# Kernel optimization log

Hardware: AMD Instinct MI355X
Metric: run time of the kernel (lower is better)

Reference implementation:

```python
import jax, jax.numpy as jnp
import numpy as np

D = 1024
H = 16
DH = D // H  # 64
EPS = 1e-5


def _ln(x, w, b=None):
    mu = jnp.mean(x, axis=-1, keepdims=True)
    var = jnp.var(x, axis=-1, keepdims=True)
    y = (x - mu) * jax.lax.rsqrt(var + EPS) * w
    return y + b if b is not None else y


def _rotate_half(x):
    x1, x2 = jnp.split(x, 2, axis=-1)
    return jnp.concatenate([-x2, x1], axis=-1)


def _rope(q, k):
    # q, k: [B, L, H, DH]; rotary over sequence dim (ESM-style half-split rotation)
    L = q.shape[1]
    inv_freq = 1.0 / (10000.0 ** (jnp.arange(0, DH, 2, dtype=jnp.float32) / DH))
    freqs = jnp.arange(L, dtype=jnp.float32)[:, None] * inv_freq[None, :]  # [L, DH/2]
    emb = jnp.concatenate([freqs, freqs], axis=-1)  # [L, DH]
    cos = jnp.cos(emb)[None, :, None, :]  # [1, L, 1, DH]
    sin = jnp.sin(emb)[None, :, None, :]
    q = q * cos + _rotate_half(q) * sin
    k = k * cos + _rotate_half(k) * sin
    return q, k


def setup_inputs() -> dict:
    key = jax.random.key(0)
    ks = jax.random.split(key, 8)
    B, L = 2, 2048
    x = jax.random.normal(ks[0], (B, L, D), dtype=jnp.float32)
    seq_id = jnp.sort(jax.random.randint(ks[1], (B, L), 0, 8), axis=-1)
    s = 1.0 / np.sqrt(D)
    return {
        "x": x,
        "seq_id": seq_id,
        "ln1_w": jnp.ones((D,), jnp.float32),
        "ln1_b": jnp.zeros((D,), jnp.float32),
        "w_qkv": jax.random.normal(ks[2], (3 * D, D), dtype=jnp.float32) * s,
        "q_ln_w": jnp.ones((D,), jnp.float32),
        "k_ln_w": jnp.ones((D,), jnp.float32),
        "out_w": jax.random.normal(ks[3], (D, D), dtype=jnp.float32) * s,
    }


def reference(x, seq_id, ln1_w, ln1_b, w_qkv, q_ln_w, k_ln_w, out_w):
    B, L, _ = x.shape
    h = _ln(x, ln1_w, ln1_b)
    qkv = jnp.einsum("bld,ed->ble", h, w_qkv)  # [B, L, 3D]
    q, k, v = jnp.split(qkv, 3, axis=-1)
    q = _ln(q, q_ln_w)
    k = _ln(k, k_ln_w)
    q = q.reshape(B, L, H, DH)
    k = k.reshape(B, L, H, DH)
    q, k = _rope(q, k)
    q = q.transpose(0, 2, 1, 3)  # [B, H, L, DH]
    k = k.transpose(0, 2, 1, 3)
    v = v.reshape(B, L, H, DH).transpose(0, 2, 1, 3)
    scale = 1.0 / np.sqrt(DH)
    scores = jnp.einsum("bhld,bhmd->bhlm", q, k) * scale  # [B, H, L, L]
    mask = (seq_id[:, None, :, None] == seq_id[:, None, None, :])  # [B, 1, L, L]
    scores = jnp.where(mask, scores, -jnp.inf)
    attn = jax.nn.softmax(scores, axis=-1)
    ctx = jnp.einsum("bhlm,bhmd->bhld", attn, v)  # [B, H, L, DH]
    ctx = ctx.transpose(0, 2, 1, 3).reshape(B, L, D)
    return jnp.einsum("bld,ed->ble", ctx, out_w)
```

## Files before the change

kernel.cpp:

```cpp
#include <hip/hip_runtime.h>
#include <hip/hip_bf16.h>
#include <math.h>

#define D 1024
#define H 16
#define DH 64
#define L 2048
#define B 2
#define NROW (B * L)
#define EPS 1e-5f

typedef _Float16 half8 __attribute__((ext_vector_type(8)));
typedef _Float16 half4v __attribute__((ext_vector_type(4)));
typedef float f32x4 __attribute__((ext_vector_type(4)));

__global__ __launch_bounds__(256) void prep_kernel(const float* __restrict__ x,
                                                   const float* __restrict__ lw,
                                                   const float* __restrict__ lb,
                                                   _Float16* __restrict__ h16,
                                                   const float* __restrict__ wqkv,
                                                   _Float16* __restrict__ wqkv16,
                                                   const float* __restrict__ outw,
                                                   _Float16* __restrict__ outw16,
                                                   const int* __restrict__ seq_id,
                                                   int* __restrict__ lo,
                                                   int* __restrict__ hi,
                                                   float2* __restrict__ rtab) {
    int blk = blockIdx.x;
    int t = threadIdx.x;
    if (blk < 4096) {
        int r = blk;
        const float* xr = x + (size_t)r * D;
        float4 v = *(const float4*)&xr[t * 4];
        float s = v.x + v.y + v.z + v.w;
        float sq = v.x * v.x + v.y * v.y + v.z * v.z + v.w * v.w;
        for (int off = 32; off > 0; off >>= 1) {
            s += __shfl_xor(s, off, 64);
            sq += __shfl_xor(sq, off, 64);
        }
        __shared__ float ls[4], lq[4];
        int wave = t >> 6;
        if ((t & 63) == 0) { ls[wave] = s; lq[wave] = sq; }
        __syncthreads();
        float S = ls[0] + ls[1] + ls[2] + ls[3];
        float Q = lq[0] + lq[1] + lq[2] + lq[3];
        float mu = S / (float)D;
        float rs = rsqrtf(Q / (float)D - mu * mu + EPS);
        float4 w4 = *(const float4*)&lw[t * 4];
        float4 b4 = *(const float4*)&lb[t * 4];
        half4v o = {(_Float16)((v.x - mu) * rs * w4.x + b4.x),
                    (_Float16)((v.y - mu) * rs * w4.y + b4.y),
                    (_Float16)((v.z - mu) * rs * w4.z + b4.z),
                    (_Float16)((v.w - mu) * rs * w4.w + b4.w)};
        *(half4v*)&h16[(size_t)r * D + t * 4] = o;
    } else if (blk < 6144) {
        int base = blk - 4096;
        const float* src;
        _Float16* dst;
        if (base < 1536) { src = wqkv; dst = wqkv16; }
        else             { src = outw; dst = outw16; base -= 1536; }
        int i = (base * 256 + t) * 8;
        float4 a = *(const float4*)&src[i];
        float4 b = *(const float4*)&src[i + 4];
        half8 h = {(_Float16)a.x, (_Float16)a.y, (_Float16)a.z, (_Float16)a.w,
                   (_Float16)b.x, (_Float16)b.y, (_Float16)b.z, (_Float16)b.w};
        *(half8*)&dst[i] = h;
    } else if (blk < 6160) {
        int idx = (blk - 6144) * 256 + t;
        int b = idx / L, l = idx - b * L;
        const int* row = seq_id + (size_t)b * L;
        int v = row[l];
        int a = 0, c = L;
        while (a < c) { int m = (a + c) >> 1; if (row[m] < v) a = m + 1; else c = m; }
        lo[idx] = a;
        a = 0; c = L;
        while (a < c) { int m = (a + c) >> 1; if (row[m] <= v) a = m + 1; else c = m; }
        hi[idx] = a;
    } else {
        int idx = (blk - 6160) * 256 + t;
        int l = idx >> 5, fi = idx & 31;
        float invf = expf(-(float)fi * 0.28782313662425572f);
        float sn, cs;
        sincosf((float)l * invf, &sn, &cs);
        rtab[idx] = make_float2(cs, sn);
    }
}

template <typename OutT, int BM, int BN>
__global__ __launch_bounds__(256) void gemm_f16_kernel(const _Float16* __restrict__ A,
                                                       const _Float16* __restrict__ W,
                                                       OutT* __restrict__ C, int N) {
    constexpr int WM = BM / 2, WN = BN / 2;
    constexpr int MT = WM / 16, NT = WN / 16;
    __shared__ _Float16 As[2][BM * 32];
    __shared__ _Float16 Bs[2][BN * 32];
    int t = threadIdx.x;
    int w = t >> 6, lane = t & 63;
    int quad = lane >> 4, col = lane & 15;
    int m0 = blockIdx.y * BM, n0 = blockIdx.x * BN;
    int mw = (w >> 1) * WM, nw = (w & 1) * WN;
    int sw = (col >> 1) & 3;

    f32x4 acc[MT][NT] = {};

    auto stage = [&](int k0, int buf) {
#pragma unroll
        for (int i = 0; i < BM / 64; i++) {
            int e = t + i * 256;
            int row = e >> 2, kc = (e & 3) ^ ((row >> 1) & 3);
            __builtin_amdgcn_global_load_lds(
                (const __attribute__((address_space(1))) void*)&A[(size_t)(m0 + row) * 1024 + k0 + kc * 8],
                (__attribute__((address_space(3))) void*)&As[buf][e * 8], 16, 0, 0);
        }
#pragma unroll
        for (int i = 0; i < BN / 64; i++) {
            int e = t + i * 256;
            int row = e >> 2, kc = (e & 3) ^ ((row >> 1) & 3);
            __builtin_amdgcn_global_load_lds(
                (const __attribute__((address_space(1))) void*)&W[(size_t)(n0 + row) * 1024 + k0 + kc * 8],
                (__attribute__((address_space(3))) void*)&Bs[buf][e * 8], 16, 0, 0);
        }
    };

    stage(0, 0);
    int cur = 0;
    for (int k0 = 0; k0 < 1024; k0 += 32) {
        __syncthreads();
        if (k0 + 32 < 1024) stage(k0 + 32, cur ^ 1);
        half8 af[MT], bf[NT];
#pragma unroll
        for (int mt = 0; mt < MT; mt++)
            af[mt] = *(const half8*)&As[cur][(mw + mt * 16 + col) * 32 + ((quad ^ sw) << 3)];
#pragma unroll
        for (int nt = 0; nt < NT; nt++)
            bf[nt] = *(const half8*)&Bs[cur][(nw + nt * 16 + col) * 32 + ((quad ^ sw) << 3)];
#pragma unroll
        for (int mt = 0; mt < MT; mt++)
#pragma unroll
            for (int nt = 0; nt < NT; nt++)
                acc[mt][nt] = __builtin_amdgcn_mfma_f32_16x16x32_f16(af[mt], bf[nt], acc[mt][nt], 0, 0, 0);
        cur ^= 1;
    }

#pragma unroll
    for (int mt = 0; mt < MT; mt++)
#pragma unroll
        for (int nt = 0; nt < NT; nt++)
#pragma unroll
            for (int r = 0; r < 4; r++) {
                int row = m0 + mw + mt * 16 + quad * 4 + r;
                int cc = n0 + nw + nt * 16 + col;
                C[(size_t)row * N + cc] = (OutT)acc[mt][nt][r];
            }
}

__global__ __launch_bounds__(256) void mid_kernel(const _Float16* __restrict__ qkv,
                                                  const float* __restrict__ qw,
                                                  const float* __restrict__ kw,
                                                  const float2* __restrict__ rtab,
                                                  _Float16* __restrict__ q_r,
                                                  _Float16* __restrict__ k_r,
                                                  _Float16* __restrict__ v_t) {
    __shared__ float ls[4], lq[4];
    __shared__ _Float16 T[64][64];
    int blk = blockIdx.x;
    int t = threadIdx.x;
    if (blk < 8192) {
        int r = blk >> 1;
        int which = blk & 1;
        const _Float16* src = qkv + (size_t)r * 3072 + which * 1024;
        const float* w = which ? kw : qw;
        _Float16* dst = which ? k_r : q_r;

        float vals[4];
        float s = 0.f, sq = 0.f;
#pragma unroll
        for (int i = 0; i < 4; i++) {
            float v = (float)src[t + i * 256];
            vals[i] = v;
            s += v;
            sq += v * v;
        }
        for (int off = 32; off > 0; off >>= 1) {
            s += __shfl_xor(s, off, 64);
            sq += __shfl_xor(sq, off, 64);
        }
        int wave = t >> 6;
        if ((t & 63) == 0) { ls[wave] = s; lq[wave] = sq; }
        __syncthreads();
        float S = ls[0] + ls[1] + ls[2] + ls[3];
        float Q = lq[0] + lq[1] + lq[2] + lq[3];
        float mu = S / 1024.f;
        float rs = rsqrtf(Q / 1024.f - mu * mu + EPS);

        int l = r & (L - 1);
        int b = r >> 11;
#pragma unroll
        for (int i = 0; i < 4; i++) {
            int j = t + i * 256;
            float y = (vals[i] - mu) * rs * w[j];
            float p = __shfl_xor(y, 32, 64);
            int dh = j & 63, hh = j >> 6;
            float2 cs = rtab[l * 32 + (dh & 31)];
            float out = (dh < 32) ? (y * cs.x - p * cs.y) : (y * cs.x + p * cs.y);
            dst[((size_t)((b * H + hh) * L + l)) * 64 + dh] = (_Float16)out;
        }
    } else {
        int vb = blk - 8192;
        int bh = vb >> 5;
        int b = bh >> 4, h = bh & 15;
        int l0 = (vb & 31) * 64;
#pragma unroll
        for (int i = 0; i < 2; i++) {
            int e = t + i * 256;
            int li = e >> 3, ch = e & 7;
            half8 hv = *(const half8*)&qkv[((size_t)(b * L + l0 + li)) * 3072 + 2048 + h * 64 + ch * 8];
            *(half8*)&T[li][((ch ^ (li >> 3)) & 7) * 8] = hv;
        }
        __syncthreads();
#pragma unroll
        for (int i = 0; i < 2; i++) {
            int e = t + i * 256;
            int d = e >> 3, ch = e & 7;
            half8 hv;
#pragma unroll
            for (int j = 0; j < 8; j++)
                hv[j] = T[ch * 8 + j][((((d >> 3) ^ ch) & 7) * 8) + (d & 7)];
            *(half8*)&v_t[((size_t)(bh * 64 + d)) * 2048 + l0 + ch * 8] = hv;
        }
    }
}

__global__ __launch_bounds__(256) void attn_mfma_kernel(const _Float16* __restrict__ q_r,
                                                        const _Float16* __restrict__ k_r,
                                                        const _Float16* __restrict__ v_t,
                                                        const int* __restrict__ lo_arr,
                                                        const int* __restrict__ hi_arr,
                                                        _Float16* __restrict__ ctx) {
    __shared__ _Float16 Ks[2][64][64];
    __shared__ _Float16 Vs[2][64][64];
    __shared__ _Float16 Ps[4][16][64];
    int bh = blockIdx.y;
    int b = bh >> 4, h = bh & 15;
    int l0 = blockIdx.x * 64;
    int t = threadIdx.x;
    int w = t >> 6, lane = t & 63;
    int quad = lane >> 4, col = lane & 15;
    int rbase = l0 + w * 16;

    int blo = lo_arr[b * L + l0] & ~63;
    int bhi = hi_arr[b * L + l0 + 63];

    auto stage = [&](int m0, int buf) {
#pragma unroll
        for (int i = 0; i < 2; i++) {
            int e = t + i * 256;
            int row = e >> 3, ch = e & 7;
            int sch = ch ^ (row & 7);
            __builtin_amdgcn_global_load_lds(
                (const __attribute__((address_space(1))) void*)&k_r[((size_t)(bh * L + m0 + row)) * 64 + sch * 8],
                (__attribute__((address_space(3))) void*)&Ks[buf][row][ch * 8], 16, 0, 0);
            __builtin_amdgcn_global_load_lds(
                (const __attribute__((address_space(1))) void*)&v_t[((size_t)(bh * 64 + row)) * 2048 + m0 + sch * 8],
                (__attribute__((address_space(3))) void*)&Vs[buf][row][ch * 8], 16, 0, 0);
        }
    };

    stage(blo, 0);

    half8 qf0, qf1;
    {
        const _Float16* qp = q_r + ((size_t)(bh * L + rbase + col)) * 64 + quad * 8;
        qf0 = *(const half8*)qp;
        qf1 = *(const half8*)(qp + 32);
    }
    int lo_c = lo_arr[b * L + rbase + col];
    int hi_c = hi_arr[b * L + rbase + col];
    int wlo = __shfl(lo_c, 15, 64);
    int whi = __shfl(hi_c, 0, 64);

    f32x4 o[4] = {};
    float m_run = -1e30f, l_run = 0.f;
    const float SCL = 0.125f * 1.4426950408889634f;
    int swz = (col & 7) << 3;
    int src = (lane & 48) | ((lane & 48) >> 2);

    int cur = 0;
    for (int m0 = blo; m0 < bhi; m0 += 64) {
        __syncthreads();
        if (m0 + 64 < bhi) stage(m0 + 64, cur ^ 1);

        f32x4 s[4] = {};
#pragma unroll
        for (int nt = 0; nt < 4; nt++) {
            int key = nt * 16 + col;
            const _Float16* kp = &Ks[cur][key][0];
            half8 kf0 = *(const half8*)&kp[(quad ^ (key & 7)) * 8];
            half8 kf1 = *(const half8*)&kp[((quad + 4) ^ (key & 7)) * 8];
            s[nt] = __builtin_amdgcn_mfma_f32_16x16x32_f16(kf0, qf0, s[nt], 0, 0, 0);
            s[nt] = __builtin_amdgcn_mfma_f32_16x16x32_f16(kf1, qf1, s[nt], 0, 0, 0);
        }

        float p[4][4];
        bool full = (m0 >= wlo) && (m0 + 64 <= whi);
        if (full) {
#pragma unroll
            for (int nt = 0; nt < 4; nt++)
#pragma unroll
                for (int r = 0; r < 4; r++) p[nt][r] = s[nt][r] * SCL;
        } else {
#pragma unroll
            for (int nt = 0; nt < 4; nt++) {
                int kb = m0 + nt * 16 + quad * 4;
#pragma unroll
                for (int r = 0; r < 4; r++) {
                    int key = kb + r;
                    p[nt][r] = (key >= lo_c && key < hi_c) ? s[nt][r] * SCL : -INFINITY;
                }
            }
        }

        float tmax = p[0][0];
#pragma unroll
        for (int nt = 0; nt < 4; nt++)
#pragma unroll
            for (int r = 0; r < 4; r++) tmax = fmaxf(tmax, p[nt][r]);
        tmax = fmaxf(tmax, __shfl_xor(tmax, 16, 64));
        tmax = fmaxf(tmax, __shfl_xor(tmax, 32, 64));
        float nm = fmaxf(m_run, tmax);
        float corr = exp2f(m_run - nm);
        m_run = nm;
        float rs = 0.f;
#pragma unroll
        for (int nt = 0; nt < 4; nt++)
#pragma unroll
            for (int r = 0; r < 4; r++) {
                float e2 = exp2f(p[nt][r] - nm);
                p[nt][r] = e2;
                rs += e2;
            }
        rs += __shfl_xor(rs, 16, 64);
        rs += __shfl_xor(rs, 32, 64);
        l_run = l_run * corr + rs;

#pragma unroll
        for (int nt = 0; nt < 4; nt++) {
            half4v pk = {(_Float16)p[nt][0], (_Float16)p[nt][1],
                         (_Float16)p[nt][2], (_Float16)p[nt][3]};
            *(half4v*)&Ps[w][col][(nt * 16 + quad * 4) ^ swz] = pk;
        }

#pragma unroll
        for (int r = 0; r < 4; r++) {
            float c4 = __shfl(corr, src + r, 64);
            o[0][r] *= c4; o[1][r] *= c4; o[2][r] *= c4; o[3][r] *= c4;
        }

        half8 pf0 = *(const half8*)&Ps[w][col][(quad * 8) ^ swz];
        half8 pf1 = *(const half8*)&Ps[w][col][(32 + quad * 8) ^ swz];
#pragma unroll
        for (int nt = 0; nt < 4; nt++) {
            int dr = nt * 16 + col;
            const _Float16* vp = &Vs[cur][dr][0];
            half8 vf0 = *(const half8*)&vp[(quad ^ (dr & 7)) * 8];
            half8 vf1 = *(const half8*)&vp[((quad + 4) ^ (dr & 7)) * 8];
            o[nt] = __builtin_amdgcn_mfma_f32_16x16x32_f16(pf0, vf0, o[nt], 0, 0, 0);
            o[nt] = __builtin_amdgcn_mfma_f32_16x16x32_f16(pf1, vf1, o[nt], 0, 0, 0);
        }
        cur ^= 1;
    }

#pragma unroll
    for (int r = 0; r < 4; r++) {
        float linv = 1.f / __shfl(l_run, src + r, 64);
        int row = rbase + quad * 4 + r;
#pragma unroll
        for (int nt = 0; nt < 4; nt++)
            ctx[((size_t)(b * L + row)) * 1024 + h * 64 + nt * 16 + col] =
                (_Float16)(o[nt][r] * linv);
    }
}

extern "C" void kernel_launch(void* const* d_in, const int* in_sizes, int n_in,
                              void* d_out, int out_size, void* d_ws, size_t ws_size,
                              hipStream_t stream) {
    const float* x      = (const float*)d_in[0];
    const int*   seq_id = (const int*)d_in[1];
    const float* ln1_w  = (const float*)d_in[2];
    const float* ln1_b  = (const float*)d_in[3];
    const float* w_qkv  = (const float*)d_in[4];
    const float* q_ln_w = (const float*)d_in[5];
    const float* k_ln_w = (const float*)d_in[6];
    const float* out_w  = (const float*)d_in[7];
    float* out = (float*)d_out;

    char* ws = (char*)d_ws;
    int*      lo     = (int*)(ws);
    int*      hi     = (int*)(ws + (64 << 10));
    float2*   rtab   = (float2*)(ws + (128 << 10));
    _Float16* h16    = (_Float16*)(ws + (1ull << 20));
    _Float16* wqkv16 = (_Float16*)(ws + (10ull << 20));
    _Float16* outw16 = (_Float16*)(ws + (17ull << 20));
    _Float16* qkv16  = (_Float16*)(ws + (20ull << 20));
    _Float16* q_r    = (_Float16*)(ws + (45ull << 20));
    _Float16* k_r    = (_Float16*)(ws + (54ull << 20));
    _Float16* v_t    = (_Float16*)(ws + (63ull << 20));
    _Float16* ctx16  = (_Float16*)(ws + (72ull << 20));

    prep_kernel<<<dim3(6416), dim3(256), 0, stream>>>(
        x, ln1_w, ln1_b, h16, w_qkv, wqkv16, out_w, outw16, seq_id, lo, hi, rtab);
    gemm_f16_kernel<_Float16, 128, 128><<<dim3(3072 / 128, NROW / 128), dim3(256), 0, stream>>>(
        h16, wqkv16, qkv16, 3072);
    mid_kernel<<<dim3(9216), dim3(256), 0, stream>>>(qkv16, q_ln_w, k_ln_w, rtab, q_r, k_r, v_t);
    attn_mfma_kernel<<<dim3(L / 64, B * H), dim3(256), 0, stream>>>(q_r, k_r, v_t, lo, hi, ctx16);
    gemm_f16_kernel<float, 128, 64><<<dim3(1024 / 64, NROW / 128), dim3(256), 0, stream>>>(
        ctx16, outw16, out, 1024);

    (void)in_sizes; (void)n_in; (void)out_size; (void)ws_size;
}
```

Measured before the change: 190.2 us.

## Remap GEMM tiles across XCDs, vectorize q/k norm-rope, enlarge attention blocks

The GEMM kernel remaps its flat block index so consecutive tiles go to the same XCD (stride-8 interleave), aiming at better L2 reuse. The q/k layernorm plus rotary kernel now handles one row's q and k per block with 8-wide vector loads and stores, using a lane shuffle of 4 for the rotate-half pairing. The attention kernel moves to 512 threads covering 128 query rows per block, so each staged K/V tile serves twice as many queries. The cost is fewer attention blocks and a wider key range per block, which means more masked work at segment boundaries.

```diff
diff --git a/kernel.cpp b/kernel.cpp
--- a/kernel.cpp
+++ b/kernel.cpp
@@ -97,7 +97,11 @@
     int t = threadIdx.x;
     int w = t >> 6, lane = t & 63;
     int quad = lane >> 4, col = lane & 15;
-    int m0 = blockIdx.y * BM, n0 = blockIdx.x * BN;
+    int nx = gridDim.x;
+    int ib = blockIdx.y * nx + blockIdx.x;
+    int nwg = nx * gridDim.y;
+    int ni = (ib & 7) * (nwg >> 3) + (ib >> 3);
+    int m0 = (ni / nx) * BM, n0 = (ni % nx) * BN;
     int mw = (w >> 1) * WM, nw = (w & 1) * WN;
     int sw = (col >> 1) & 3;
 
@@ -165,19 +169,21 @@
     __shared__ _Float16 T[64][64];
     int blk = blockIdx.x;
     int t = threadIdx.x;
-    if (blk < 8192) {
-        int r = blk >> 1;
-        int which = blk & 1;
-        const _Float16* src = qkv + (size_t)r * 3072 + which * 1024;
-        const float* w = which ? kw : qw;
-        _Float16* dst = which ? k_r : q_r;
-
-        float vals[4];
+    if (blk < 4096) {
+        int r = blk;
+        int half = t >> 7;
+        int tt = t & 127;
+        const _Float16* src = qkv + (size_t)r * 3072 + half * 1024;
+        const float* wgt = half ? kw : qw;
+        _Float16* dst = half ? k_r : q_r;
+
+        half8 hv = *(const half8*)&src[tt * 8];
+        float y[8];
         float s = 0.f, sq = 0.f;
 #pragma unroll
-        for (int i = 0; i < 4; i++) {
-            float v = (float)src[t + i * 256];
-            vals[i] = v;
+        for (int e = 0; e < 8; e++) {
+            float v = (float)hv[e];
+            y[e] = v;
             s += v;
             sq += v * v;
         }
@@ -188,25 +194,37 @@
         int wave = t >> 6;
         if ((t & 63) == 0) { ls[wave] = s; lq[wave] = sq; }
         __syncthreads();
-        float S = ls[0] + ls[1] + ls[2] + ls[3];
-        float Q = lq[0] + lq[1] + lq[2] + lq[3];
+        int base = half << 1;
+        float S = ls[base] + ls[base + 1];
+        float Q = lq[base] + lq[base + 1];
         float mu = S / 1024.f;
         float rs = rsqrtf(Q / 1024.f - mu * mu + EPS);
 
         int l = r & (L - 1);
         int b = r >> 11;
-#pragma unroll
-        for (int i = 0; i < 4; i++) {
-            int j = t + i * 256;
-            float y = (vals[i] - mu) * rs * w[j];
-            float p = __shfl_xor(y, 32, 64);
-            int dh = j & 63, hh = j >> 6;
-            float2 cs = rtab[l * 32 + (dh & 31)];
-            float out = (dh < 32) ? (y * cs.x - p * cs.y) : (y * cs.x + p * cs.y);
-            dst[((size_t)((b * H + hh) * L + l)) * 64 + dh] = (_Float16)out;
-        }
+        int j0 = tt * 8;
+        int dh0 = j0 & 63, hh = j0 >> 6;
+        const float2* cp = &rtab[l * 32 + (dh0 & 31)];
+        float4 c01 = *(const float4*)cp;
+        float4 c23 = *(const float4*)(cp + 2);
+        float4 c45 = *(const float4*)(cp + 4);
+        float4 c67 = *(const float4*)(cp + 6);
+        float cs_[8] = {c01.x, c01.z, c23.x, c23.z, c45.x, c45.z, c67.x, c67.z};
+        float sn_[8] = {c01.y, c01.w, c23.y, c23.w, c45.y, c45.w, c67.y, c67.w};
+
+        float yn[8];
+#pragma unroll
+        for (int e = 0; e < 8; e++) yn[e] = (y[e] - mu) * rs * wgt[j0 + e];
+        float sgn = (dh0 < 32) ? -1.f : 1.f;
+        half8 o;
+#pragma unroll
+        for (int e = 0; e < 8; e++) {
+            float p = __shfl_xor(yn[e], 4, 64);
+            o[e] = (_Float16)(yn[e] * cs_[e] + sgn * p * sn_[e]);
+        }
+        *(half8*)&dst[((size_t)((b * H + hh) * L + l)) * 64 + dh0] = o;
     } else {
-        int vb = blk - 8192;
+        int vb = blk - 4096;
         int bh = vb >> 5;
         int b = bh >> 4, h = bh & 15;
         int l0 = (vb & 31) * 64;
@@ -231,7 +249,7 @@
     }
 }
 
-__global__ __launch_bounds__(256) void attn_mfma_kernel(const _Float16* __restrict__ q_r,
+__global__ __launch_bounds__(512) void attn_mfma_kernel(const _Float16* __restrict__ q_r,
                                                         const _Float16* __restrict__ k_r,
                                                         const _Float16* __restrict__ v_t,
                                                         const int* __restrict__ lo_arr,
@@ -239,31 +257,27 @@
                                                         _Float16* __restrict__ ctx) {
     __shared__ _Float16 Ks[2][64][64];
     __shared__ _Float16 Vs[2][64][64];
-    __shared__ _Float16 Ps[4][16][64];
+    __shared__ _Float16 Ps[8][16][64];
     int bh = blockIdx.y;
     int b = bh >> 4, h = bh & 15;
-    int l0 = blockIdx.x * 64;
+    int l0 = blockIdx.x * 128;
     int t = threadIdx.x;
     int w = t >> 6, lane = t & 63;
     int quad = lane >> 4, col = lane & 15;
     int rbase = l0 + w * 16;
 
     int blo = lo_arr[b * L + l0] & ~63;
-    int bhi = hi_arr[b * L + l0 + 63];
+    int bhi = hi_arr[b * L + l0 + 127];
 
     auto stage = [&](int m0, int buf) {
-#pragma unroll
-        for (int i = 0; i < 2; i++) {
-            int e = t + i * 256;
-            int row = e >> 3, ch = e & 7;
-            int sch = ch ^ (row & 7);
-            __builtin_amdgcn_global_load_lds(
-                (const __attribute__((address_space(1))) void*)&k_r[((size_t)(bh * L + m0 + row)) * 64 + sch * 8],
-                (__attribute__((address_space(3))) void*)&Ks[buf][row][ch * 8], 16, 0, 0);
-            __builtin_amdgcn_global_load_lds(
-                (const __attribute__((address_space(1))) void*)&v_t[((size_t)(bh * 64 + row)) * 2048 + m0 + sch * 8],
-                (__attribute__((address_space(3))) void*)&Vs[buf][row][ch * 8], 16, 0, 0);
-        }
+        int row = t >> 3, ch = t & 7;
+        int sch = ch ^ (row & 7);
+        __builtin_amdgcn_global_load_lds(
+            (const __attribute__((address_space(1))) void*)&k_r[((size_t)(bh * L + m0 + row)) * 64 + sch * 8],
+            (__attribute__((address_space(3))) void*)&Ks[buf][row][ch * 8], 16, 0, 0);
+        __builtin_amdgcn_global_load_lds(
+            (const __attribute__((address_space(1))) void*)&v_t[((size_t)(bh * 64 + row)) * 2048 + m0 + sch * 8],
+            (__attribute__((address_space(3))) void*)&Vs[buf][row][ch * 8], 16, 0, 0);
     };
 
     stage(blo, 0);
@@ -411,8 +425,8 @@
         x, ln1_w, ln1_b, h16, w_qkv, wqkv16, out_w, outw16, seq_id, lo, hi, rtab);
     gemm_f16_kernel<_Float16, 128, 128><<<dim3(3072 / 128, NROW / 128), dim3(256), 0, stream>>>(
         h16, wqkv16, qkv16, 3072);
-    mid_kernel<<<dim3(9216), dim3(256), 0, stream>>>(qkv16, q_ln_w, k_ln_w, rtab, q_r, k_r, v_t);
-    attn_mfma_kernel<<<dim3(L / 64, B * H), dim3(256), 0, stream>>>(q_r, k_r, v_t, lo, hi, ctx16);
+    mid_kernel<<<dim3(5120), dim3(256), 0, stream>>>(qkv16, q_ln_w, k_ln_w, rtab, q_r, k_r, v_t);
+    attn_mfma_kernel<<<dim3(L / 128, B * H), dim3(512), 0, stream>>>(q_r, k_r, v_t, lo, hi, ctx16);
     gemm_f16_kernel<float, 128, 64><<<dim3(1024 / 64, NROW / 128), dim3(256), 0, stream>>>(
         ctx16, outw16, out, 1024);
 
```

After: 185.1 us. -2.7%, faster.
